# Optimization experiments

Hardware: AMD Instinct MI355X
Metric: run time of the kernel (lower is better)

## Reference

```python
import jax, jax.numpy as jnp
import numpy as np

NUM_USERS = 100000
NUM_POIS = 50000
N = NUM_USERS + NUM_POIS   # total graph nodes (users then pois)
D = 128                    # embedding_dim
POI_D = 320                # poi_embed_dim
E = 2000000                # number of edges
B = 1024                   # batch of user ids
NEG_SLOPE = 0.2


def setup_inputs() -> dict:
    key = jax.random.key(0)
    ks = jax.random.split(key, 12)
    stdv = 1.0 / np.sqrt(D)  # module resets all params to U(-stdv, stdv)
    u = lambda k, s: jax.random.uniform(k, s, jnp.float32, -stdv, stdv)
    return {
        "user_idx": jax.random.randint(ks[0], (B,), 0, NUM_USERS),
        "poi_embeddings": jax.random.normal(ks[1], (NUM_POIS, POI_D), jnp.float32),
        "edge_index": jax.random.randint(ks[2], (2, E), 0, N),
        "user_table": u(ks[3], (NUM_USERS, D)),
        "Wp": u(ks[4], (POI_D, D)), "bp": u(ks[5], (D,)),
        "W1": u(ks[6], (D, D)), "b1": u(ks[7], (D,)),
        "W2": u(ks[8], (D, D)), "b2": u(ks[9], (D,)),
        "Wf": u(ks[10], (D, D)), "bf": u(ks[11], (D,)),
    }


def _leaky(x):
    return jnp.where(x >= 0, x, NEG_SLOPE * x)


def _gcn_conv(x, W, b, src, dst, dinv):
    # PyG GCNConv: h = xW; out_i = sum_{j->i} dinv_j*dinv_i*h_j + dinv_i^2*h_i + b
    h = x @ W
    norm = dinv[src] * dinv[dst]                       # [E]
    agg = jax.ops.segment_sum(h[src] * norm[:, None], dst, num_segments=N)
    agg = agg + (dinv * dinv)[:, None] * h             # self-loop term
    return agg + b


def reference(user_idx, poi_embeddings, edge_index, user_table,
              Wp, bp, W1, b1, W2, b2, Wf, bf):
    src, dst = edge_index[0], edge_index[1]
    # degree with self-loops (edge weight 1)
    deg = 1.0 + jax.ops.segment_sum(jnp.ones((E,), jnp.float32), dst, num_segments=N)
    dinv = jax.lax.rsqrt(deg)

    poi_feats = poi_embeddings @ Wp + bp               # [NUM_POIS, D]
    x = jnp.concatenate([user_table, poi_feats], axis=0)  # [N, D]
    x = _leaky(_gcn_conv(x, W1, b1, src, dst, dinv))
    # dropout p=0.2 is identity in eval mode
    x = _leaky(_gcn_conv(x, W2, b2, src, dst, dinv))

    out = x[user_idx] + user_table[user_idx]           # [B, D]
    return out @ Wf + bf
```

## Files before the change

kernel.cpp:

```cpp
#include <hip/hip_runtime.h>

#define NUSERS 100000
#define NPOIS  50000
#define NN     150000
#define DD     128
#define EE     2000000
#define BB     1024
#define NT2M   32768

#define CH_IPT 16
#define CH_BLK 256
#define CHUNK  (CH_IPT * CH_BLK)

#define HR   3
#define HS   50000
#define HSI  12500
#define HC   85
#define HPER 23532

typedef __attribute__((ext_vector_type(8))) short short8;
typedef __attribute__((ext_vector_type(4))) float f32x4;
typedef unsigned short ushort_t;

__device__ __forceinline__ ushort_t f2bf(float x) {
    union { float f; unsigned u; } a; a.f = x;
    unsigned r = a.u + 0x7fffu + ((a.u >> 16) & 1u);
    return (ushort_t)(r >> 16);
}
__device__ __forceinline__ float bf2f(ushort_t h) {
    union { unsigned u; float f; } a; a.u = ((unsigned)h) << 16;
    return a.f;
}

__global__ void k_mark(const int* __restrict__ uidx, int* __restrict__ mask_s2,
                       int* __restrict__ mask_t2) {
    int b = blockIdx.x * blockDim.x + threadIdx.x;
    if (b < BB) { int u = uidx[b]; mask_s2[u] = 1; mask_t2[u] = 1; }
}

__global__ void k_markT2(const int* __restrict__ src, const int* __restrict__ dst,
                         const int* __restrict__ mask_s2, int* __restrict__ mask_t2) {
    const int nq = EE / 4;
    int stride = gridDim.x * blockDim.x;
    for (int q = blockIdx.x * blockDim.x + threadIdx.x; q < nq; q += stride) {
        int4 d4 = *(const int4*)&dst[q << 2];
        int m0 = mask_s2[d4.x], m1 = mask_s2[d4.y];
        int m2 = mask_s2[d4.z], m3 = mask_s2[d4.w];
        if (m0 | m1 | m2 | m3) {
            int4 s4 = *(const int4*)&src[q << 2];
            if (m0) mask_t2[s4.x] = 1;
            if (m1) mask_t2[s4.y] = 1;
            if (m2) mask_t2[s4.z] = 1;
            if (m3) mask_t2[s4.w] = 1;
        }
    }
}

__global__ __launch_bounds__(1024)
void k_hist3(const int* __restrict__ dst, int* __restrict__ slab) {
    __shared__ int h[HSI];
    const int r = blockIdx.x / HC, c = blockIdx.x % HC;
    const int lo = r * HS;
    const int tid = threadIdx.x;
    for (int i = tid; i < HSI; i += 1024) h[i] = 0;
    __syncthreads();
    const int e0 = c * HPER;
    const int e1 = min(e0 + HPER, EE);
    for (int e = e0 + tid * 4; e < e1; e += 4096) {
        int4 d4 = *(const int4*)&dst[e];
        unsigned u0 = (unsigned)(d4.x - lo), u1 = (unsigned)(d4.y - lo);
        unsigned u2 = (unsigned)(d4.z - lo), u3 = (unsigned)(d4.w - lo);
        if (u0 < (unsigned)HS) atomicAdd(&h[u0 >> 2], 1 << ((u0 & 3) << 3));
        if (u1 < (unsigned)HS) atomicAdd(&h[u1 >> 2], 1 << ((u1 & 3) << 3));
        if (u2 < (unsigned)HS) atomicAdd(&h[u2 >> 2], 1 << ((u2 & 3) << 3));
        if (u3 < (unsigned)HS) atomicAdd(&h[u3 >> 2], 1 << ((u3 & 3) << 3));
    }
    __syncthreads();
    int* out = slab + (size_t)blockIdx.x * HSI;
    for (int i = tid; i < HSI; i += 1024) out[i] = h[i];
}

__global__ void k_reduce3(const int* __restrict__ slab, int* __restrict__ cnt,
                          float* __restrict__ dinv) {
    int i = blockIdx.x * blockDim.x + threadIdx.x;
    if (i >= HR * HSI) return;
    int r = i / HSI, ii = i - r * HSI;
    const int* p = slab + (size_t)(r * HC) * HSI + ii;
    int s = 0;
    #pragma unroll
    for (int c = 0; c < HC; ++c) s += p[(size_t)c * HSI];
    int n0 = r * HS + (ii << 2);
    int4 cv;
    cv.x = s & 255; cv.y = (s >> 8) & 255; cv.z = (s >> 16) & 255; cv.w = (s >> 24) & 255;
    *(int4*)&cnt[n0] = cv;
    float4 dv;
    dv.x = rsqrtf(1.0f + (float)cv.x); dv.y = rsqrtf(1.0f + (float)cv.y);
    dv.z = rsqrtf(1.0f + (float)cv.z); dv.w = rsqrtf(1.0f + (float)cv.w);
    *(float4*)&dinv[n0] = dv;
}

__global__ __launch_bounds__(256)
void k_slots(const int* __restrict__ mask_s2, const int* __restrict__ mask_t2,
             int* __restrict__ slot_s2, int* __restrict__ slot_t2,
             int* __restrict__ rev_s2, int* __restrict__ rev_t2,
             int* __restrict__ ctr) {
    __shared__ int s_wcnt_t[4], s_wcnt_s[4];
    __shared__ int s_base_t, s_base_s;
    const int tid = threadIdx.x;
    const int lane = tid & 63;
    const int wid = tid >> 6;
    const int nch = (NN + CHUNK - 1) / CHUNK;
    for (int c = blockIdx.x; c < nch; c += gridDim.x) {
        const int n0 = c * CHUNK;
        unsigned hbits_t = 0, hbits_s = 0;
        int wt = 0, ws = 0;
        #pragma unroll
        for (int i = 0; i < CH_IPT; ++i) {
            int n = n0 + i * CH_BLK + tid;
            bool inb = (n < NN);
            bool ht = inb && (mask_t2[n] != 0);
            bool hs = inb && (mask_s2[n] != 0);
            unsigned long long mt = __ballot(ht);
            unsigned long long ms = __ballot(hs);
            if (ht) hbits_t |= (1u << i);
            if (hs) hbits_s |= (1u << i);
            wt += __popcll(mt); ws += __popcll(ms);
        }
        if (lane == 0) { s_wcnt_t[wid] = wt; s_wcnt_s[wid] = ws; }
        __syncthreads();
        if (tid == 0) s_base_t = atomicAdd(&ctr[0], s_wcnt_t[0]+s_wcnt_t[1]+s_wcnt_t[2]+s_wcnt_t[3]);
        if (tid == 1) s_base_s = atomicAdd(&ctr[1], s_wcnt_s[0]+s_wcnt_s[1]+s_wcnt_s[2]+s_wcnt_s[3]);
        __syncthreads();
        int off_t = s_base_t, off_s = s_base_s;
        for (int w = 0; w < wid; ++w) { off_t += s_wcnt_t[w]; off_s += s_wcnt_s[w]; }
        #pragma unroll
        for (int i = 0; i < CH_IPT; ++i) {
            unsigned long long mt = __ballot((hbits_t >> i) & 1);
            unsigned long long ms = __ballot((hbits_s >> i) & 1);
            int n = n0 + i * CH_BLK + tid;
            if ((hbits_t >> i) & 1) {
                int p = off_t + __popcll(mt & ((1ull << lane) - 1ull));
                slot_t2[n] = p; rev_t2[p] = n;
            }
            if ((hbits_s >> i) & 1) {
                int p = off_s + __popcll(ms & ((1ull << lane) - 1ull));
                slot_s2[n] = p; rev_s2[p] = n;
            }
            off_t += __popcll(mt); off_s += __popcll(ms);
        }
        __syncthreads();
    }
}

__global__ __launch_bounds__(1024)
void k_scan2(const int* __restrict__ ctr, const int* __restrict__ rev_t2,
             const int* __restrict__ rev_s2, const int* __restrict__ cnt,
             int* __restrict__ ptr1, int* __restrict__ cur1,
             int* __restrict__ ptr2, int* __restrict__ cur2) {
    __shared__ int wsum[16];
    __shared__ int s_carry;
    const int which = blockIdx.x;
    const int n = ctr[which];
    const int* rev = which ? rev_s2 : rev_t2;
    int* ptr = which ? ptr2 : ptr1;
    int* cur = which ? cur2 : cur1;
    const int tid = threadIdx.x;
    const int lane = tid & 63, wid = tid >> 6;
    if (tid == 0) s_carry = 0;
    __syncthreads();
    for (int base = 0; base < n; base += 4096) {
        int i0 = base + tid * 4;
        int v[4];
        #pragma unroll
        for (int k = 0; k < 4; ++k) {
            int i = i0 + k;
            v[k] = (i < n) ? cnt[rev[i]] : 0;
        }
        int tsum = v[0] + v[1] + v[2] + v[3];
        int x = tsum;
        #pragma unroll
        for (int s = 1; s < 64; s <<= 1) {
            int y = __shfl_up(x, s, 64);
            if (lane >= s) x += y;
        }
        if (lane == 63) wsum[wid] = x;
        __syncthreads();
        if (wid == 0) {
            int wv = (lane < 16) ? wsum[lane] : 0;
            #pragma unroll
            for (int s = 1; s < 16; s <<= 1) {
                int y = __shfl_up(wv, s, 64);
                if (lane >= s) wv += y;
            }
            if (lane < 16) wsum[lane] = wv;
        }
        __syncthreads();
        int carry = s_carry;
        int woff = (wid > 0) ? wsum[wid - 1] : 0;
        int excl = carry + woff + (x - tsum);
        #pragma unroll
        for (int k = 0; k < 4; ++k) {
            int i = i0 + k;
            if (i < n) { ptr[i] = excl; cur[i] = excl; }
            excl += v[k];
        }
        __syncthreads();
        if (tid == 0) s_carry = carry + wsum[15];
        __syncthreads();
    }
}

__global__ void k_scatter(const int* __restrict__ src, const int* __restrict__ dst,
                          const int* __restrict__ mask_s2, const int* __restrict__ mask_t2,
                          const int* __restrict__ slot_s2, const int* __restrict__ slot_t2,
                          int* __restrict__ cur1, int* __restrict__ cur2,
                          int* __restrict__ csr1, int* __restrict__ csr2) {
    int stride = gridDim.x * blockDim.x;
    for (int e = blockIdx.x * blockDim.x + threadIdx.x; e < EE; e += stride) {
        int d = dst[e];
        bool t = (mask_t2[d] != 0);
        bool s2 = (mask_s2[d] != 0);
        if (t | s2) {
            int s = src[e];
            if (t)  { int p = atomicAdd(&cur1[slot_t2[d]], 1); csr1[p] = s; }
            if (s2) { int p = atomicAdd(&cur2[slot_s2[d]], 1); csr2[p] = s; }
        }
    }
}

__global__ void k_wpw1(const float* __restrict__ Wp, const float* __restrict__ W1,
                       float* __restrict__ WpW1) {
    int i = blockIdx.x * blockDim.x + threadIdx.x;
    if (i >= 320 * 128) return;
    int r = i >> 7, c = i & 127;
    float s = 0.f;
    for (int k = 0; k < 128; ++k) s = fmaf(Wp[r * 128 + k], W1[k * 128 + c], s);
    WpW1[i] = s;
}

__global__ void k_bpw1(const float* __restrict__ bp, const float* __restrict__ W1,
                       float* __restrict__ bpW1) {
    int c = threadIdx.x;
    float s = 0.f;
    for (int k = 0; k < 128; ++k) s = fmaf(bp[k], W1[k * 128 + c], s);
    bpW1[c] = s;
}

__global__ void k_wprepW(const float* __restrict__ W1, const float* __restrict__ WpW1,
                         const float* __restrict__ bpW1,
                         ushort_t* __restrict__ Th, ushort_t* __restrict__ Tl) {
    int i = blockIdx.x * blockDim.x + threadIdx.x;
    if (i >= 128 * 512) return;
    int n = i >> 9, k = i & 511;
    float x = (k < 128) ? W1[k * 128 + n]
            : (k < 448) ? WpW1[(k - 128) * 128 + n]
            : (k == 448) ? bpW1[n] : 0.f;
    ushort_t h = f2bf(x);
    ushort_t l = f2bf(x - bf2f(h));
    Th[n * 512 + k] = h; Tl[n * 512 + k] = l;
}

__global__ void k_wprep2(const float* __restrict__ W2, const float* __restrict__ Wf,
                         ushort_t* __restrict__ T2h, ushort_t* __restrict__ T2l,
                         ushort_t* __restrict__ Tfh, ushort_t* __restrict__ Tfl) {
    int i = blockIdx.x * blockDim.x + threadIdx.x;
    if (i >= 2 * 128 * 128) return;
    int wsel = i >> 14, j = i & 16383;
    const float* W = wsel ? Wf : W2;
    ushort_t* Th = wsel ? Tfh : T2h;
    ushort_t* Tl = wsel ? Tfl : T2l;
    int k = j >> 7, n = j & 127;
    float x = W[j];
    ushort_t h = f2bf(x);
    ushort_t l = f2bf(x - bf2f(h));
    Th[n * 128 + k] = h; Tl[n * 128 + k] = l;
}

__global__ __launch_bounds__(256)
void k_agg1(const int* __restrict__ ctr, const int* __restrict__ rev_t2,
            const int* __restrict__ ptr1, const int* __restrict__ cnt,
            const int* __restrict__ csr1, const float* __restrict__ dinv,
            const float* __restrict__ ut, const float* __restrict__ poi,
            ushort_t* __restrict__ Ah, ushort_t* __restrict__ Al) {
    const int nt2 = min(ctr[0], NT2M);
    const int lane = threadIdx.x & 63;
    const int w0 = (blockIdx.x * blockDim.x + threadIdx.x) >> 6;
    const int nw = (gridDim.x * blockDim.x) >> 6;
    for (int slot = w0; slot < nt2; slot += nw) {
        int node = rev_t2[slot];
        float dn = dinv[node], dd = dn * dn;
        float u0 = 0.f, u1 = 0.f, p0 = 0.f, p1 = 0.f, p2 = 0.f, p3 = 0.f, p4 = 0.f, sP = 0.f;
        if (node < NUSERS) {
            const float2 v = *(const float2*)&ut[((size_t)node << 7) + (lane << 1)];
            u0 = dd * v.x; u1 = dd * v.y;
        } else {
            const float* pr = poi + (size_t)(node - NUSERS) * 320;
            p0 = dd * pr[lane]; p1 = dd * pr[lane + 64]; p2 = dd * pr[lane + 128];
            p3 = dd * pr[lane + 192]; p4 = dd * pr[lane + 256];
            sP = dd;
        }
        int j = ptr1[slot], jend = j + cnt[node];
        for (; j < jend; ++j) {
            int s = csr1[j];
            float w = dinv[s] * dn;
            if (s < NUSERS) {
                const float2 v = *(const float2*)&ut[((size_t)s << 7) + (lane << 1)];
                u0 = fmaf(w, v.x, u0); u1 = fmaf(w, v.y, u1);
            } else {
                const float* pr = poi + (size_t)(s - NUSERS) * 320;
                p0 = fmaf(w, pr[lane], p0); p1 = fmaf(w, pr[lane + 64], p1);
                p2 = fmaf(w, pr[lane + 128], p2); p3 = fmaf(w, pr[lane + 192], p3);
                p4 = fmaf(w, pr[lane + 256], p4);
                sP += w;
            }
        }
        size_t base = (size_t)slot << 9;
        ushort_t h, l;
        h = f2bf(u0); l = f2bf(u0 - bf2f(h));
        Ah[base + (lane << 1)] = h; Al[base + (lane << 1)] = l;
        h = f2bf(u1); l = f2bf(u1 - bf2f(h));
        Ah[base + (lane << 1) + 1] = h; Al[base + (lane << 1) + 1] = l;
        float pv[5] = {p0, p1, p2, p3, p4};
        #pragma unroll
        for (int q = 0; q < 5; ++q) {
            h = f2bf(pv[q]); l = f2bf(pv[q] - bf2f(h));
            Ah[base + 128 + lane + (q << 6)] = h; Al[base + 128 + lane + (q << 6)] = l;
        }
        float t = (lane == 0) ? sP : 0.f;
        h = f2bf(t); l = f2bf(t - bf2f(h));
        Ah[base + 448 + lane] = h; Al[base + 448 + lane] = l;
    }
}

template<int KSTEPS, bool LEAKY>
__global__ __launch_bounds__(256)
void gemm_bf(const ushort_t* __restrict__ Ah_g, const ushort_t* __restrict__ Al_g,
             const ushort_t* __restrict__ BTh, const ushort_t* __restrict__ BTl,
             const float* __restrict__ bias, float* __restrict__ C,
             int M, const int* __restrict__ Mdyn)
{
    constexpr int K = KSTEPS * 64;
    __shared__ ushort_t Bh[128 * 64], Bl[128 * 64];
    __shared__ ushort_t Ahs[64 * 64], Als[64 * 64];
    const int tid = threadIdx.x;
    const int wave = tid >> 6, lane = tid & 63;
    const int wr = wave >> 1, wc = wave & 1;
    const int lr = lane & 15, g = lane >> 4;
    if (Mdyn) M = min(*Mdyn, NT2M);
    const int ntiles = (M + 63) >> 6;
    for (int tile = blockIdx.x; tile < ntiles; tile += gridDim.x) {
        const int row0 = tile << 6;
        f32x4 acc[2][4];
        #pragma unroll
        for (int a = 0; a < 2; ++a)
            #pragma unroll
            for (int b = 0; b < 4; ++b) acc[a][b] = (f32x4){0.f, 0.f, 0.f, 0.f};
        for (int kc = 0; kc < K; kc += 64) {
            __syncthreads();
            #pragma unroll
            for (int i = 0; i < 4; ++i) {
                int c = tid + i * 256;
                int n = c >> 3, kq = c & 7;
                size_t go = (size_t)n * K + kc + kq * 8;
                int boff = n * 128 + ((kq * 16) ^ ((n & 7) << 4));
                *(int4*)((char*)Bh + boff) = *(const int4*)&BTh[go];
                *(int4*)((char*)Bl + boff) = *(const int4*)&BTl[go];
            }
            #pragma unroll
            for (int i = 0; i < 2; ++i) {
                int c = tid + i * 256;
                int r = c >> 3, kq = c & 7;
                int row = row0 + r;
                int4 va = {0, 0, 0, 0}, vb = {0, 0, 0, 0};
                if (row < M) {
                    size_t go = (size_t)row * K + kc + kq * 8;
                    va = *(const int4*)&Ah_g[go];
                    vb = *(const int4*)&Al_g[go];
                }
                int aoff = r * 128 + ((kq * 16) ^ ((r & 7) << 4));
                *(int4*)((char*)Ahs + aoff) = va;
                *(int4*)((char*)Als + aoff) = vb;
            }
            __syncthreads();
            #pragma unroll
            for (int kk2 = 0; kk2 < 2; ++kk2) {
                short8 afh[2], afl[2];
                #pragma unroll
                for (int rt = 0; rt < 2; ++rt) {
                    int ar = wr * 32 + rt * 16 + lr;
                    int off = ar * 128 + ((kk2 * 64 + g * 16) ^ ((ar & 7) << 4));
                    afh[rt] = *(short8*)((char*)Ahs + off);
                    afl[rt] = *(short8*)((char*)Als + off);
                }
                #pragma unroll
                for (int ct = 0; ct < 4; ++ct) {
                    int bn = wc * 64 + ct * 16 + lr;
                    int off = bn * 128 + ((kk2 * 64 + g * 16) ^ ((bn & 7) << 4));
                    short8 bfh = *(short8*)((char*)Bh + off);
                    short8 bfl = *(short8*)((char*)Bl + off);
                    #pragma unroll
                    for (int rt = 0; rt < 2; ++rt) {
                        acc[rt][ct] = __builtin_amdgcn_mfma_f32_16x16x32_bf16(afh[rt], bfh, acc[rt][ct], 0, 0, 0);
                        acc[rt][ct] = __builtin_amdgcn_mfma_f32_16x16x32_bf16(afh[rt], bfl, acc[rt][ct], 0, 0, 0);
                        acc[rt][ct] = __builtin_amdgcn_mfma_f32_16x16x32_bf16(afl[rt], bfh, acc[rt][ct], 0, 0, 0);
                    }
                }
            }
        }
        #pragma unroll
        for (int ct = 0; ct < 4; ++ct) {
            int col = wc * 64 + ct * 16 + lr;
            float bv = bias[col];
            #pragma unroll
            for (int rt = 0; rt < 2; ++rt) {
                #pragma unroll
                for (int v = 0; v < 4; ++v) {
                    int row = row0 + wr * 32 + rt * 16 + g * 4 + v;
                    if (row < M) {
                        float o = acc[rt][ct][v] + bv;
                        if (LEAKY) o = o >= 0.f ? o : 0.2f * o;
                        C[(size_t)row * 128 + col] = o;
                    }
                }
            }
        }
    }
}

__global__ __launch_bounds__(256)
void k_agg2(const int* __restrict__ ctr, const int* __restrict__ rev_s2,
            const int* __restrict__ ptr2, const int* __restrict__ cnt,
            const int* __restrict__ csr2, const int* __restrict__ slot_t2,
            const float* __restrict__ dinv, const float* __restrict__ x1c,
            ushort_t* __restrict__ X2h, ushort_t* __restrict__ X2l) {
    const int ns2 = ctr[1];
    const int lane = threadIdx.x & 63;
    const int col = lane << 1;
    const int w0 = (blockIdx.x * blockDim.x + threadIdx.x) >> 6;
    const int nw = (gridDim.x * blockDim.x) >> 6;
    for (int slot = w0; slot < ns2; slot += nw) {
        int node = rev_s2[slot];
        float dn = dinv[node], dd = dn * dn;
        float2 acc = *(const float2*)&x1c[((size_t)slot_t2[node] << 7) + col];
        acc.x *= dd; acc.y *= dd;
        int j = ptr2[slot], jend = j + cnt[node];
        for (; j < jend; ++j) {
            int s = csr2[j];
            float w = dinv[s] * dn;
            const float2 h = *(const float2*)&x1c[((size_t)slot_t2[s] << 7) + col];
            acc.x = fmaf(w, h.x, acc.x);
            acc.y = fmaf(w, h.y, acc.y);
        }
        size_t base = ((size_t)slot << 7) + col;
        ushort_t h0 = f2bf(acc.x), l0 = f2bf(acc.x - bf2f(h0));
        ushort_t h1 = f2bf(acc.y), l1 = f2bf(acc.y - bf2f(h1));
        X2h[base] = h0; X2h[base + 1] = h1;
        X2l[base] = l0; X2l[base + 1] = l1;
    }
}

__global__ void k_finalA(const int* __restrict__ uidx, const int* __restrict__ slot_s2,
                         const float* __restrict__ x2c, const float* __restrict__ ut,
                         ushort_t* __restrict__ Fh, ushort_t* __restrict__ Fl) {
    int i = blockIdx.x * blockDim.x + threadIdx.x;
    if (i >= BB * 64) return;
    int b = i >> 6, l = i & 63;
    int u = uidx[b];
    const float2 xv = *(const float2*)&x2c[((size_t)slot_s2[u] << 7) + (l << 1)];
    const float2 uv = *(const float2*)&ut[((size_t)u << 7) + (l << 1)];
    float a0 = xv.x + uv.x, a1 = xv.y + uv.y;
    size_t base = ((size_t)b << 7) + (l << 1);
    ushort_t h0 = f2bf(a0), l0 = f2bf(a0 - bf2f(h0));
    ushort_t h1 = f2bf(a1), l1 = f2bf(a1 - bf2f(h1));
    Fh[base] = h0; Fh[base + 1] = h1;
    Fl[base] = l0; Fl[base + 1] = l1;
}

extern "C" void kernel_launch(void* const* d_in, const int* in_sizes, int n_in,
                              void* d_out, int out_size, void* d_ws, size_t ws_size,
                              hipStream_t stream) {
    const int*   uidx    = (const int*)d_in[0];
    const float* poi     = (const float*)d_in[1];
    const int*   src     = (const int*)d_in[2];
    const int*   dst     = ((const int*)d_in[2]) + EE;
    const float* usert   = (const float*)d_in[3];
    const float* Wp      = (const float*)d_in[4];
    const float* bp      = (const float*)d_in[5];
    const float* W1      = (const float*)d_in[6];
    const float* b1      = (const float*)d_in[7];
    const float* W2      = (const float*)d_in[8];
    const float* b2      = (const float*)d_in[9];
    const float* Wf      = (const float*)d_in[10];
    const float* bf      = (const float*)d_in[11];
    float* out = (float*)d_out;

    char* w = (char*)d_ws;
    size_t off = 0;
    auto alloc = [&](size_t bytes) -> void* {
        void* p = w + off;
        off = (off + bytes + 255) & ~(size_t)255;
        return p;
    };
    float* dinv    = (float*)alloc((size_t)NN * 4);
    int*   cnt     = (int*)  alloc((size_t)NN * 4);
    int*   mask_s2 = (int*)  alloc((size_t)NN * 4);
    int*   mask_t2 = (int*)  alloc((size_t)NN * 4);
    int*   slot_s2 = (int*)  alloc((size_t)NN * 4);
    int*   slot_t2 = (int*)  alloc((size_t)NN * 4);
    int*   rev_t2  = (int*)  alloc((size_t)NN * 4);
    int*   rev_s2  = (int*)  alloc((size_t)BB * 4);
    int*   ptr1    = (int*)  alloc((size_t)(NN + 1) * 4);
    int*   cur1    = (int*)  alloc((size_t)(NN + 1) * 4);
    int*   ptr2    = (int*)  alloc((size_t)(BB + 2) * 4);
    int*   cur2    = (int*)  alloc((size_t)(BB + 2) * 4);
    int*   ctr     = (int*)  alloc(256);
    int*   csr1    = (int*)  alloc((size_t)EE * 4);
    int*   csr2    = (int*)  alloc((size_t)EE * 4);
    int*   slab    = (int*)  alloc((size_t)HR * HC * HSI * 4);
    float* WpW1    = (float*)alloc((size_t)320 * 128 * 4);
    float* bpW1    = (float*)alloc((size_t)128 * 4);
    ushort_t* WTh  = (ushort_t*)alloc((size_t)128 * 512 * 2);
    ushort_t* WTl  = (ushort_t*)alloc((size_t)128 * 512 * 2);
    ushort_t* W2Th = (ushort_t*)alloc((size_t)128 * 128 * 2);
    ushort_t* W2Tl = (ushort_t*)alloc((size_t)128 * 128 * 2);
    ushort_t* WfTh = (ushort_t*)alloc((size_t)128 * 128 * 2);
    ushort_t* WfTl = (ushort_t*)alloc((size_t)128 * 128 * 2);
    ushort_t* Ah   = (ushort_t*)alloc((size_t)NT2M * 512 * 2);
    ushort_t* Al   = (ushort_t*)alloc((size_t)NT2M * 512 * 2);
    float* x1c     = (float*)alloc((size_t)NT2M * 128 * 4);
    ushort_t* X2h  = (ushort_t*)alloc((size_t)2048 * 128 * 2);
    ushort_t* X2l  = (ushort_t*)alloc((size_t)2048 * 128 * 2);
    float* x2c     = (float*)alloc((size_t)2048 * 128 * 4);
    ushort_t* Fh   = (ushort_t*)alloc((size_t)BB * 128 * 2);
    ushort_t* Fl   = (ushort_t*)alloc((size_t)BB * 128 * 2);
    if (off > ws_size) return;

    hipMemsetAsync(mask_s2, 0, (size_t)NN * 4, stream);
    hipMemsetAsync(mask_t2, 0, (size_t)NN * 4, stream);
    hipMemsetAsync(ctr, 0, 256, stream);

    k_wpw1  <<<160, 256, 0, stream>>>(Wp, W1, WpW1);
    k_bpw1  <<<1, 128, 0, stream>>>(bp, W1, bpW1);
    k_wprepW<<<256, 256, 0, stream>>>(W1, WpW1, bpW1, WTh, WTl);
    k_wprep2<<<128, 256, 0, stream>>>(W2, Wf, W2Th, W2Tl, WfTh, WfTl);

    k_mark   <<<(BB + 255) / 256, 256, 0, stream>>>(uidx, mask_s2, mask_t2);
    k_markT2 <<<2048, 256, 0, stream>>>(src, dst, mask_s2, mask_t2);
    k_hist3  <<<HR * HC, 1024, 0, stream>>>(dst, slab);
    k_reduce3<<<(HR * HSI + 255) / 256, 256, 0, stream>>>(slab, cnt, dinv);

    k_slots<<<(NN + CHUNK - 1) / CHUNK, 256, 0, stream>>>(mask_s2, mask_t2, slot_s2, slot_t2,
                                                          rev_s2, rev_t2, ctr);
    k_scan2<<<2, 1024, 0, stream>>>(ctr, rev_t2, rev_s2, cnt, ptr1, cur1, ptr2, cur2);
    k_scatter<<<2048, 256, 0, stream>>>(src, dst, mask_s2, mask_t2, slot_s2, slot_t2,
                                        cur1, cur2, csr1, csr2);

    k_agg1<<<2048, 256, 0, stream>>>(ctr, rev_t2, ptr1, cnt, csr1, dinv, usert, poi, Ah, Al);
    gemm_bf<8, true><<<240, 256, 0, stream>>>(Ah, Al, WTh, WTl, b1, x1c, 0, ctr + 0);

    k_agg2<<<256, 256, 0, stream>>>(ctr, rev_s2, ptr2, cnt, csr2, slot_t2, dinv, x1c, X2h, X2l);
    gemm_bf<2, true><<<16, 256, 0, stream>>>(X2h, X2l, W2Th, W2Tl, b2, x2c, 0, ctr + 1);

    k_finalA<<<(BB * 64 + 255) / 256, 256, 0, stream>>>(uidx, slot_s2, x2c, usert, Fh, Fl);
    gemm_bf<2, false><<<16, 256, 0, stream>>>(Fh, Fl, WfTh, WfTl, bf, out, BB, nullptr);
}
```

Baseline: 217.9 us.

## Partition CSR neighbors by user/POI type and unroll gather loops

The CSR scatter now fills user sources from the front of each node's segment and POI sources from the back, using a second cursor that counts down. The layer-1 aggregation can then run separate branch-free loops over the user and POI neighbors, unrolled by 4 and 2 so several row gathers are in flight at once. Layer-2 aggregation also gets a 4-way unrolled gather loop. The intent is to remove per-edge divergence and raise memory-level parallelism, at the cost of an extra cursor array and more atomics state in the scatter.

Result: faster. 195.7 us (-10.2%).

```diff
diff --git a/kernel.cpp b/kernel.cpp
--- a/kernel.cpp
+++ b/kernel.cpp
@@ -155,8 +155,8 @@
 __global__ __launch_bounds__(1024)
 void k_scan2(const int* __restrict__ ctr, const int* __restrict__ rev_t2,
              const int* __restrict__ rev_s2, const int* __restrict__ cnt,
-             int* __restrict__ ptr1, int* __restrict__ cur1,
-             int* __restrict__ ptr2, int* __restrict__ cur2) {
+             int* __restrict__ ptr1, int* __restrict__ cur1, int* __restrict__ cur1b,
+             int* __restrict__ ptr2, int* __restrict__ cur2, int* __restrict__ cur2b) {
     __shared__ int wsum[16];
     __shared__ int s_carry;
     const int which = blockIdx.x;
@@ -164,6 +164,7 @@
     const int* rev = which ? rev_s2 : rev_t2;
     int* ptr = which ? ptr2 : ptr1;
     int* cur = which ? cur2 : cur1;
+    int* curB = which ? cur2b : cur1b;
     const int tid = threadIdx.x;
     const int lane = tid & 63, wid = tid >> 6;
     if (tid == 0) s_carry = 0;
@@ -201,7 +202,7 @@
         #pragma unroll
         for (int k = 0; k < 4; ++k) {
             int i = i0 + k;
-            if (i < n) { ptr[i] = excl; cur[i] = excl; }
+            if (i < n) { ptr[i] = excl; cur[i] = excl; curB[i] = excl + v[k]; }
             excl += v[k];
         }
         __syncthreads();
@@ -213,7 +214,8 @@
 __global__ void k_scatter(const int* __restrict__ src, const int* __restrict__ dst,
                           const int* __restrict__ mask_s2, const int* __restrict__ mask_t2,
                           const int* __restrict__ slot_s2, const int* __restrict__ slot_t2,
-                          int* __restrict__ cur1, int* __restrict__ cur2,
+                          int* __restrict__ cur1, int* __restrict__ cur1b,
+                          int* __restrict__ cur2,
                           int* __restrict__ csr1, int* __restrict__ csr2) {
     int stride = gridDim.x * blockDim.x;
     for (int e = blockIdx.x * blockDim.x + threadIdx.x; e < EE; e += stride) {
@@ -222,7 +224,11 @@
         bool s2 = (mask_s2[d] != 0);
         if (t | s2) {
             int s = src[e];
-            if (t)  { int p = atomicAdd(&cur1[slot_t2[d]], 1); csr1[p] = s; }
+            if (t) {
+                int sl = slot_t2[d];
+                if (s < NUSERS) { int p = atomicAdd(&cur1[sl], 1);  csr1[p] = s; }
+                else            { int p = atomicAdd(&cur1b[sl], -1); csr1[p - 1] = s; }
+            }
             if (s2) { int p = atomicAdd(&cur2[slot_s2[d]], 1); csr2[p] = s; }
         }
     }
@@ -278,8 +284,9 @@
 
 __global__ __launch_bounds__(256)
 void k_agg1(const int* __restrict__ ctr, const int* __restrict__ rev_t2,
-            const int* __restrict__ ptr1, const int* __restrict__ cnt,
-            const int* __restrict__ csr1, const float* __restrict__ dinv,
+            const int* __restrict__ ptr1, const int* __restrict__ cur1,
+            const int* __restrict__ cnt, const int* __restrict__ csr1,
+            const float* __restrict__ dinv,
             const float* __restrict__ ut, const float* __restrict__ poi,
             ushort_t* __restrict__ Ah, ushort_t* __restrict__ Al) {
     const int nt2 = min(ctr[0], NT2M);
@@ -299,20 +306,50 @@
             p3 = dd * pr[lane + 192]; p4 = dd * pr[lane + 256];
             sP = dd;
         }
-        int j = ptr1[slot], jend = j + cnt[node];
+        const int j0 = ptr1[slot];
+        const int sp = cur1[slot];
+        const int jend = j0 + cnt[node];
+        int j = j0;
+        for (; j + 4 <= sp; j += 4) {
+            int s0 = csr1[j], s1 = csr1[j + 1], s2 = csr1[j + 2], s3 = csr1[j + 3];
+            float w0 = dinv[s0] * dn, w1 = dinv[s1] * dn;
+            float w2 = dinv[s2] * dn, w3 = dinv[s3] * dn;
+            const float2 v0 = *(const float2*)&ut[((size_t)s0 << 7) + (lane << 1)];
+            const float2 v1 = *(const float2*)&ut[((size_t)s1 << 7) + (lane << 1)];
+            const float2 v2 = *(const float2*)&ut[((size_t)s2 << 7) + (lane << 1)];
+            const float2 v3 = *(const float2*)&ut[((size_t)s3 << 7) + (lane << 1)];
+            u0 = fmaf(w0, v0.x, u0); u1 = fmaf(w0, v0.y, u1);
+            u0 = fmaf(w1, v1.x, u0); u1 = fmaf(w1, v1.y, u1);
+            u0 = fmaf(w2, v2.x, u0); u1 = fmaf(w2, v2.y, u1);
+            u0 = fmaf(w3, v3.x, u0); u1 = fmaf(w3, v3.y, u1);
+        }
+        for (; j < sp; ++j) {
+            int s = csr1[j];
+            float w = dinv[s] * dn;
+            const float2 v = *(const float2*)&ut[((size_t)s << 7) + (lane << 1)];
+            u0 = fmaf(w, v.x, u0); u1 = fmaf(w, v.y, u1);
+        }
+        for (j = sp; j + 2 <= jend; j += 2) {
+            int s0 = csr1[j], s1 = csr1[j + 1];
+            float w0 = dinv[s0] * dn, w1 = dinv[s1] * dn;
+            const float* pa = poi + (size_t)(s0 - NUSERS) * 320;
+            const float* pb = poi + (size_t)(s1 - NUSERS) * 320;
+            p0 = fmaf(w0, pa[lane], p0);       p1 = fmaf(w0, pa[lane + 64], p1);
+            p2 = fmaf(w0, pa[lane + 128], p2); p3 = fmaf(w0, pa[lane + 192], p3);
+            p4 = fmaf(w0, pa[lane + 256], p4);
+            p0 = fmaf(w1, pb[lane], p0);       p1 = fmaf(w1, pb[lane + 64], p1);
+            p2 = fmaf(w1, pb[lane + 128], p2); p3 = fmaf(w1, pb[lane + 192], p3);
+            p4 = fmaf(w1, pb[lane + 256], p4);
+            sP += w0 + w1;
+        }
         for (; j < jend; ++j) {
             int s = csr1[j];
             float w = dinv[s] * dn;
-            if (s < NUSERS) {
-                const float2 v = *(const float2*)&ut[((size_t)s << 7) + (lane << 1)];
-                u0 = fmaf(w, v.x, u0); u1 = fmaf(w, v.y, u1);
-            } else {
-                const float* pr = poi + (size_t)(s - NUSERS) * 320;
-                p0 = fmaf(w, pr[lane], p0); p1 = fmaf(w, pr[lane + 64], p1);
-                p2 = fmaf(w, pr[lane + 128], p2); p3 = fmaf(w, pr[lane + 192], p3);
-                p4 = fmaf(w, pr[lane + 256], p4);
-                sP += w;
-            }
+            const float* pr = poi + (size_t)(s - NUSERS) * 320;
+            p0 = fmaf(w, pr[lane], p0);       p1 = fmaf(w, pr[lane + 64], p1);
+            p2 = fmaf(w, pr[lane + 128], p2); p3 = fmaf(w, pr[lane + 192], p3);
+            p4 = fmaf(w, pr[lane + 256], p4);
+            sP += w;
         }
         size_t base = (size_t)slot << 9;
         ushort_t h, l;
@@ -443,7 +480,22 @@
         float dn = dinv[node], dd = dn * dn;
         float2 acc = *(const float2*)&x1c[((size_t)slot_t2[node] << 7) + col];
         acc.x *= dd; acc.y *= dd;
-        int j = ptr2[slot], jend = j + cnt[node];
+        const int j0 = ptr2[slot];
+        const int jend = j0 + cnt[node];
+        int j = j0;
+        for (; j + 4 <= jend; j += 4) {
+            int s0 = csr2[j], s1 = csr2[j + 1], s2 = csr2[j + 2], s3 = csr2[j + 3];
+            float w0 = dinv[s0] * dn, w1 = dinv[s1] * dn;
+            float w2 = dinv[s2] * dn, w3 = dinv[s3] * dn;
+            const float2 h0 = *(const float2*)&x1c[((size_t)slot_t2[s0] << 7) + col];
+            const float2 h1 = *(const float2*)&x1c[((size_t)slot_t2[s1] << 7) + col];
+            const float2 h2 = *(const float2*)&x1c[((size_t)slot_t2[s2] << 7) + col];
+            const float2 h3 = *(const float2*)&x1c[((size_t)slot_t2[s3] << 7) + col];
+            acc.x = fmaf(w0, h0.x, acc.x); acc.y = fmaf(w0, h0.y, acc.y);
+            acc.x = fmaf(w1, h1.x, acc.x); acc.y = fmaf(w1, h1.y, acc.y);
+            acc.x = fmaf(w2, h2.x, acc.x); acc.y = fmaf(w2, h2.y, acc.y);
+            acc.x = fmaf(w3, h3.x, acc.x); acc.y = fmaf(w3, h3.y, acc.y);
+        }
         for (; j < jend; ++j) {
             int s = csr2[j];
             float w = dinv[s] * dn;
@@ -511,8 +563,10 @@
     int*   rev_s2  = (int*)  alloc((size_t)BB * 4);
     int*   ptr1    = (int*)  alloc((size_t)(NN + 1) * 4);
     int*   cur1    = (int*)  alloc((size_t)(NN + 1) * 4);
+    int*   cur1b   = (int*)  alloc((size_t)(NN + 1) * 4);
     int*   ptr2    = (int*)  alloc((size_t)(BB + 2) * 4);
     int*   cur2    = (int*)  alloc((size_t)(BB + 2) * 4);
+    int*   cur2b   = (int*)  alloc((size_t)(BB + 2) * 4);
     int*   ctr     = (int*)  alloc(256);
     int*   csr1    = (int*)  alloc((size_t)EE * 4);
     int*   csr2    = (int*)  alloc((size_t)EE * 4);
@@ -551,11 +605,13 @@
 
     k_slots<<<(NN + CHUNK - 1) / CHUNK, 256, 0, stream>>>(mask_s2, mask_t2, slot_s2, slot_t2,
                                                           rev_s2, rev_t2, ctr);
-    k_scan2<<<2, 1024, 0, stream>>>(ctr, rev_t2, rev_s2, cnt, ptr1, cur1, ptr2, cur2);
+    k_scan2<<<2, 1024, 0, stream>>>(ctr, rev_t2, rev_s2, cnt,
+                                    ptr1, cur1, cur1b, ptr2, cur2, cur2b);
     k_scatter<<<2048, 256, 0, stream>>>(src, dst, mask_s2, mask_t2, slot_s2, slot_t2,
-                                        cur1, cur2, csr1, csr2);
-
-    k_agg1<<<2048, 256, 0, stream>>>(ctr, rev_t2, ptr1, cnt, csr1, dinv, usert, poi, Ah, Al);
+                                        cur1, cur1b, cur2, csr1, csr2);
+
+    k_agg1<<<2048, 256, 0, stream>>>(ctr, rev_t2, ptr1, cur1, cnt, csr1, dinv,
+                                     usert, poi, Ah, Al);
     gemm_bf<8, true><<<240, 256, 0, stream>>>(Ah, Al, WTh, WTl, b1, x1c, 0, ctr + 0);
 
     k_agg2<<<256, 256, 0, stream>>>(ctr, rev_s2, ptr2, cnt, csr2, slot_t2, dinv, x1c, X2h, X2l);
```
